# Optimization experiments

Measured on AMD Instinct MI355X. Metric: run time of the kernel, lower is better.

The kernel has to match this reference:

```python
import jax, jax.numpy as jnp
import numpy as np

N_QUBITS = 10
N_LAYERS = 4
DIM = 1 << N_QUBITS            # 1024
N3 = 3 * N_QUBITS              # params per rotation layer
N_PARAM = N3 * (N_LAYERS + 1)  # 150
BATCH = 8192

_C64 = jnp.complex64


def _rx(t):
    c = jnp.cos(t / 2).astype(_C64)
    s = jnp.sin(t / 2).astype(_C64)
    return jnp.stack([jnp.stack([c, -1j * s]), jnp.stack([-1j * s, c])])


def _ry(t):
    c = jnp.cos(t / 2).astype(_C64)
    s = jnp.sin(t / 2).astype(_C64)
    return jnp.stack([jnp.stack([c, -s]), jnp.stack([s, c])])


def _rz(t):
    e = jnp.exp(-1j * t.astype(_C64) / 2)
    z = jnp.zeros((), _C64)
    return jnp.stack([jnp.stack([e, z]), jnp.stack([z, jnp.conj(e)])])


def _apply1(state, gate, wire):
    """Apply a 2x2 gate to qubit `wire` of state [B, 2, ..., 2]."""
    axis = wire + 1  # axis 0 is batch
    s = jnp.moveaxis(state, axis, -1)
    s = jnp.einsum('ij,...j->...i', gate, s)
    return jnp.moveaxis(s, -1, axis)


def _cnot(state, ctrl, tgt):
    a, b = ctrl + 1, tgt + 1
    s = jnp.moveaxis(state, (a, b), (-2, -1))  # [..., ctrl, tgt]
    s = jnp.stack([s[..., 0, :], s[..., 1, ::-1]], axis=-2)
    return jnp.moveaxis(s, (-2, -1), (a, b))


def setup_inputs() -> dict:
    key = jax.random.key(0)
    k1, k2 = jax.random.split(key)
    x = jax.random.normal(k1, (BATCH, DIM), dtype=jnp.float32)
    he_std = (2.0 ** 0.5) * (5.0 ** -0.5)  # gain * 5^-0.5, w_mul with lrmul=1
    weight = jax.random.uniform(k2, (N_PARAM,), minval=0.0,
                                maxval=2.0 * np.pi, dtype=jnp.float32) * he_std
    return {"x": x, "weight": weight}


def reference(x, weight):
    # encoding layer: L2-normalize then cast to complex amplitudes
    norm = jnp.linalg.norm(x, axis=-1, keepdims=True)
    s = (x / jnp.maximum(norm, 1e-12)).astype(_C64)
    s = s.reshape((x.shape[0],) + (2,) * N_QUBITS)

    for l in range(N_LAYERS):
        w = weight[l * N3:(l + 1) * N3]
        # XYZ layer: Rx, then Ry, then Rz on every qubit
        for q in range(N_QUBITS):
            s = _apply1(s, _rx(w[q]), q)
        for q in range(N_QUBITS):
            s = _apply1(s, _ry(w[N_QUBITS + q]), q)
        for q in range(N_QUBITS):
            s = _apply1(s, _rz(w[2 * N_QUBITS + q]), q)
        # ring of CNOTs
        for q in range(N_QUBITS):
            s = _cnot(s, q, (q + 1) % N_QUBITS)

    # final YZY layer
    w = weight[N_LAYERS * N3:]
    for q in range(N_QUBITS):
        s = _apply1(s, _ry(w[q]), q)
    for q in range(N_QUBITS):
        s = _apply1(s, _rz(w[N_QUBITS + q]), q)
    for q in range(N_QUBITS):
        s = _apply1(s, _ry(w[2 * N_QUBITS + q]), q)

    return s.reshape(x.shape[0], 1, DIM).real
```

## Files before the change

kernel.cpp:

```cpp
#include <hip/hip_runtime.h>
#include <stdint.h>

typedef uint16_t u16;
typedef __attribute__((ext_vector_type(2))) float f32x2;
typedef __attribute__((ext_vector_type(4))) float f32x4;
typedef __attribute__((ext_vector_type(8))) short short8;
typedef __attribute__((ext_vector_type(4))) float float4v;
typedef __attribute__((ext_vector_type(4))) uint16_t u16x4;
typedef __attribute__((ext_vector_type(8))) uint16_t u16x8;

#define DIMQ 1024
#define BATCH 8192
#define KDIM 1024
#define NDIM 1024

#define RDL(v, l) __int_as_float(__builtin_amdgcn_readlane(__float_as_int(v), (l)))

__device__ __forceinline__ u16 f2bf(float f) {
  uint32_t u = __float_as_uint(f);
  u += 0x7fffu + ((u >> 16) & 1u);
  return (u16)(u >> 16);
}

template<int MASK>
__device__ __forceinline__ float lane_xor(float x) {
  if constexpr (MASK == 1)
    return __int_as_float(__builtin_amdgcn_update_dpp(0, __float_as_int(x), 0xB1, 0xF, 0xF, true));
  else if constexpr (MASK == 2)
    return __int_as_float(__builtin_amdgcn_update_dpp(0, __float_as_int(x), 0x4E, 0xF, 0xF, true));
  else if constexpr (MASK == 8)
    return __int_as_float(__builtin_amdgcn_update_dpp(0, __float_as_int(x), 0x128, 0xF, 0xF, true));
  else if constexpr (MASK == 4)
    return __int_as_float(__builtin_amdgcn_ds_swizzle(__float_as_int(x), 0x101F));
  else if constexpr (MASK == 16)
    return __int_as_float(__builtin_amdgcn_ds_swizzle(__float_as_int(x), 0x401F));
  else
    return __shfl_xor(x, 32, 64);
}

template<int MASK>
__device__ __forceinline__ void lane_gate8(float* ar, float* ai, int lane,
    float u00r, float u00i, float u01r, float u01i,
    float u10r, float u10i, float u11r, float u11i) {
  bool hi = (lane & MASK) != 0;
  float cmr = hi ? u11r : u00r, cmi = hi ? u11i : u00i;
  float cor = hi ? u10r : u01r, coi = hi ? u10i : u01i;
  float otr[8], oti[8];
#pragma unroll
  for (int r = 0; r < 8; ++r) otr[r] = lane_xor<MASK>(ar[r]);
#pragma unroll
  for (int r = 0; r < 8; ++r) oti[r] = lane_xor<MASK>(ai[r]);
#pragma unroll
  for (int k = 0; k < 4; ++k) {
    f32x2 A = {ar[2*k], ar[2*k+1]}, I = {ai[2*k], ai[2*k+1]};
    f32x2 R = {otr[2*k], otr[2*k+1]}, J = {oti[2*k], oti[2*k+1]};
    f32x2 nr = A*cmr - I*cmi + R*cor - J*coi;
    f32x2 ni = I*cmr + A*cmi + J*cor + R*coi;
    ar[2*k] = nr[0]; ar[2*k+1] = nr[1];
    ai[2*k] = ni[0]; ai[2*k+1] = ni[1];
  }
}

__device__ __forceinline__ void bfly2(f32x2 &a0r, f32x2 &a0i, f32x2 &a1r, f32x2 &a1i,
    float u00r, float u00i, float u01r, float u01i,
    float u10r, float u10i, float u11r, float u11i) {
  f32x2 t0r = a0r*u00r - a0i*u00i + a1r*u01r - a1i*u01i;
  f32x2 t0i = a0i*u00r + a0r*u00i + a1i*u01r + a1r*u01i;
  f32x2 t1r = a0r*u10r - a0i*u10i + a1r*u11r - a1i*u11i;
  f32x2 t1i = a0i*u10r + a0r*u10i + a1i*u11r + a1r*u11i;
  a0r = t0r; a0i = t0i; a1r = t1r; a1i = t1i;
}

__device__ inline void cmul2x2(float* O, const float* A, const float* B) {
  for (int r = 0; r < 2; ++r)
    for (int c = 0; c < 2; ++c) {
      float re = 0.f, im = 0.f;
      for (int j = 0; j < 2; ++j) {
        float ar = A[(r*2+j)*2], ai = A[(r*2+j)*2+1];
        float br = B[(j*2+c)*2], bi = B[(j*2+c)*2+1];
        re += ar*br - ai*bi;
        im += ar*bi + ai*br;
      }
      O[(r*2+c)*2]   = re;
      O[(r*2+c)*2+1] = im;
    }
}
__device__ inline void mk_rx(float* m, float t) {
  float s, c; sincosf(0.5f*t, &s, &c);
  m[0]=c; m[1]=0; m[2]=0; m[3]=-s; m[4]=0; m[5]=-s; m[6]=c; m[7]=0;
}
__device__ inline void mk_ry(float* m, float t) {
  float s, c; sincosf(0.5f*t, &s, &c);
  m[0]=c; m[1]=0; m[2]=-s; m[3]=0; m[4]=s; m[5]=0; m[6]=c; m[7]=0;
}
__device__ inline void mk_rz(float* m, float t) {
  float s, c; sincosf(0.5f*t, &s, &c);
  m[0]=c; m[1]=-s; m[2]=0; m[3]=0; m[4]=0; m[5]=0; m[6]=c; m[7]=s;
}

__device__ __forceinline__ int padi(int y) { return y + (y >> 4); }

__device__ __forceinline__ void do_stage(int gbase, float (&ar)[8], float (&ai)[8],
    f32x2* __restrict__ slab,
    const int (&Y)[8],
    int wbase, int lane, int h, int l4,
    float O0, float O1, float O2, float O3,
    float O4, float O5, float O6, float O7) {
#pragma unroll
  for (int j = 0; j < 8; ++j) slab[wbase + j] = (f32x2){ar[j], ai[j]};
  __syncthreads();
  {
    const int g6 = gbase + 6, g1 = gbase + 1;
    float u6r0 = h ? RDL(O4,g6) : RDL(O0,g6), u6i0 = h ? RDL(O5,g6) : RDL(O1,g6);
    float u6r1 = h ? RDL(O6,g6) : RDL(O2,g6), u6i1 = h ? RDL(O7,g6) : RDL(O3,g6);
    float u1r0 = l4 ? RDL(O4,g1) : RDL(O0,g1), u1i0 = l4 ? RDL(O5,g1) : RDL(O1,g1);
    float u1r1 = l4 ? RDL(O6,g1) : RDL(O2,g1), u1i1 = l4 ? RDL(O7,g1) : RDL(O3,g1);
    float KR[4], KI[4];
    KR[0] = u6r0*u1r0 - u6i0*u1i0;  KI[0] = u6r0*u1i0 + u6i0*u1r0;
    KR[1] = u6r0*u1r1 - u6i0*u1i1;  KI[1] = u6r0*u1i1 + u6i0*u1r1;
    KR[2] = u6r1*u1r0 - u6i1*u1i0;  KI[2] = u6r1*u1i0 + u6i1*u1r0;
    KR[3] = u6r1*u1r1 - u6i1*u1i1;  KI[3] = u6r1*u1i1 + u6i1*u1r1;
    const int CC[4] = {0, 1023, 527, 496};
    f32x2 v[8][4];
#pragma unroll
    for (int j = 0; j < 8; ++j)
#pragma unroll
      for (int m = 0; m < 4; ++m)
        v[j][m] = slab[padi(Y[j] ^ CC[m])];
#pragma unroll
    for (int k = 0; k < 4; ++k) {
      f32x2 nr = {0.f, 0.f}, ni = {0.f, 0.f};
#pragma unroll
      for (int m = 0; m < 4; ++m) {
        f32x2 Vr = {v[2*k][m][0], v[2*k+1][m][0]};
        f32x2 Vi = {v[2*k][m][1], v[2*k+1][m][1]};
        nr += Vr*KR[m] - Vi*KI[m];
        ni += Vi*KR[m] + Vr*KI[m];
      }
      ar[2*k] = nr[0]; ar[2*k+1] = nr[1];
      ai[2*k] = ni[0]; ai[2*k+1] = ni[1];
    }
  }
  { int g = gbase + 7;
    float u0r=RDL(O0,g),u0i=RDL(O1,g),u1r=RDL(O2,g),u1i=RDL(O3,g);
    float u2r=RDL(O4,g),u2i=RDL(O5,g),u3r=RDL(O6,g),u3i=RDL(O7,g);
    f32x2 a0r={ar[0],ar[1]}, a0i={ai[0],ai[1]}, a1r={ar[4],ar[5]}, a1i={ai[4],ai[5]};
    bfly2(a0r,a0i,a1r,a1i, u0r,u0i,u1r,u1i,u2r,u2i,u3r,u3i);
    ar[0]=a0r[0];ar[1]=a0r[1];ai[0]=a0i[0];ai[1]=a0i[1];
    ar[4]=a1r[0];ar[5]=a1r[1];ai[4]=a1i[0];ai[5]=a1i[1];
    f32x2 b0r={ar[2],ar[3]}, b0i={ai[2],ai[3]}, b1r={ar[6],ar[7]}, b1i={ai[6],ai[7]};
    bfly2(b0r,b0i,b1r,b1i, u0r,u0i,u1r,u1i,u2r,u2i,u3r,u3i);
    ar[2]=b0r[0];ar[3]=b0r[1];ai[2]=b0i[0];ai[3]=b0i[1];
    ar[6]=b1r[0];ar[7]=b1r[1];ai[6]=b1i[0];ai[7]=b1i[1];
  }
  { int g = gbase + 8;
    float u0r=RDL(O0,g),u0i=RDL(O1,g),u1r=RDL(O2,g),u1i=RDL(O3,g);
    float u2r=RDL(O4,g),u2i=RDL(O5,g),u3r=RDL(O6,g),u3i=RDL(O7,g);
    f32x2 a0r={ar[0],ar[1]}, a0i={ai[0],ai[1]}, a1r={ar[2],ar[3]}, a1i={ai[2],ai[3]};
    bfly2(a0r,a0i,a1r,a1i, u0r,u0i,u1r,u1i,u2r,u2i,u3r,u3i);
    ar[0]=a0r[0];ar[1]=a0r[1];ai[0]=a0i[0];ai[1]=a0i[1];
    ar[2]=a1r[0];ar[3]=a1r[1];ai[2]=a1i[0];ai[3]=a1i[1];
    f32x2 b0r={ar[4],ar[5]}, b0i={ai[4],ai[5]}, b1r={ar[6],ar[7]}, b1i={ai[6],ai[7]};
    bfly2(b0r,b0i,b1r,b1i, u0r,u0i,u1r,u1i,u2r,u2i,u3r,u3i);
    ar[4]=b0r[0];ar[5]=b0r[1];ai[4]=b0i[0];ai[5]=b0i[1];
    ar[6]=b1r[0];ar[7]=b1r[1];ai[6]=b1i[0];ai[7]=b1i[1];
  }
  { int g = gbase + 9;
    float u0r=RDL(O0,g),u0i=RDL(O1,g),u1r=RDL(O2,g),u1i=RDL(O3,g);
    float u2r=RDL(O4,g),u2i=RDL(O5,g),u3r=RDL(O6,g),u3i=RDL(O7,g);
    f32x2 a0r={ar[0],ar[2]}, a0i={ai[0],ai[2]}, a1r={ar[1],ar[3]}, a1i={ai[1],ai[3]};
    bfly2(a0r,a0i,a1r,a1i, u0r,u0i,u1r,u1i,u2r,u2i,u3r,u3i);
    ar[0]=a0r[0];ar[2]=a0r[1];ai[0]=a0i[0];ai[2]=a0i[1];
    ar[1]=a1r[0];ar[3]=a1r[1];ai[1]=a1i[0];ai[3]=a1i[1];
    f32x2 b0r={ar[4],ar[6]}, b0i={ai[4],ai[6]}, b1r={ar[5],ar[7]}, b1i={ai[5],ai[7]};
    bfly2(b0r,b0i,b1r,b1i, u0r,u0i,u1r,u1i,u2r,u2i,u3r,u3i);
    ar[4]=b0r[0];ar[6]=b0r[1];ai[4]=b0i[0];ai[6]=b0i[1];
    ar[5]=b1r[0];ar[7]=b1r[1];ai[5]=b1i[0];ai[7]=b1i[1];
  }
  { int g = gbase + 0; lane_gate8<32>(ar, ai, lane, RDL(O0,g),RDL(O1,g),RDL(O2,g),RDL(O3,g),RDL(O4,g),RDL(O5,g),RDL(O6,g),RDL(O7,g)); }
  { int g = gbase + 2; lane_gate8< 8>(ar, ai, lane, RDL(O0,g),RDL(O1,g),RDL(O2,g),RDL(O3,g),RDL(O4,g),RDL(O5,g),RDL(O6,g),RDL(O7,g)); }
  { int g = gbase + 3; lane_gate8< 4>(ar, ai, lane, RDL(O0,g),RDL(O1,g),RDL(O2,g),RDL(O3,g),RDL(O4,g),RDL(O5,g),RDL(O6,g),RDL(O7,g)); }
  { int g = gbase + 4; lane_gate8< 2>(ar, ai, lane, RDL(O0,g),RDL(O1,g),RDL(O2,g),RDL(O3,g),RDL(O4,g),RDL(O5,g),RDL(O6,g),RDL(O7,g)); }
  { int g = gbase + 5; lane_gate8< 1>(ar, ai, lane, RDL(O0,g),RDL(O1,g),RDL(O2,g),RDL(O3,g),RDL(O4,g),RDL(O5,g),RDL(O6,g),RDL(O7,g)); }
}

__global__ __launch_bounds__(256) void fused_front(const float* __restrict__ x,
                                                   const float* __restrict__ w,
                                                   u16* __restrict__ Abf,
                                                   u16* __restrict__ Bmat) {
  __shared__ f32x2 slab[2][2][1088];
  const int bid = blockIdx.x;
  const int lane = threadIdx.x & 63, wv = threadIdx.x >> 6;

  if (bid >= 512) {
    int base = (bid - 512) * 16 + wv * 4;
    for (int it = 0; it < 4; ++it) {
      int row = base + it;
      const float* xr = x + (size_t)row * DIMQ;
      float4v v[4];
      float ss = 0.f;
#pragma unroll
      for (int j = 0; j < 4; ++j) {
        v[j] = *(const float4v*)(xr + j*256 + lane*4);
        ss += v[j][0]*v[j][0] + v[j][1]*v[j][1] + v[j][2]*v[j][2] + v[j][3]*v[j][3];
      }
#pragma unroll
      for (int off = 32; off; off >>= 1) ss += __shfl_xor(ss, off, 64);
      float inv = 1.0f / fmaxf(sqrtf(ss), 1e-12f);
      u16* orow = Abf + (size_t)row * DIMQ;
#pragma unroll
      for (int j = 0; j < 4; ++j) {
        u16x4 o;
#pragma unroll
        for (int e = 0; e < 4; ++e) o[e] = f2bf(v[j][e] * inv);
        *(u16x4*)(orow + j*256 + lane*4) = o;
      }
    }
    return;
  }

  const int s = wv >> 1, h = wv & 1;
  const int l4 = (lane >> 4) & 1;
  const int d = bid * 2 + s;

  float O0, O1, O2, O3, O4, O5, O6, O7;
  {
    float A[8], B[8], C[8], T8[8], O[8];
    int t = lane;
    if (t < 50) {
      if (t < 10) {
        mk_ry(A, -w[120 + t]);
        mk_rz(B, -w[130 + t]);
        mk_ry(C, -w[140 + t]);
      } else {
        int sg = (t - 10) / 10, q = (t - 10) % 10, l = 3 - sg;
        mk_rx(A, -w[l*30 + q]);
        mk_ry(B, -w[l*30 + 10 + q]);
        mk_rz(C, -w[l*30 + 20 + q]);
      }
      cmul2x2(T8, A, B);
      cmul2x2(O, T8, C);
    } else {
#pragma unroll
      for (int j = 0; j < 8; ++j) O[j] = 0.f;
    }
    O0=O[0]; O1=O[1]; O2=O[2]; O3=O[3]; O4=O[4]; O5=O[5]; O6=O[6]; O7=O[7];
  }

  int Y[8];
#pragma unroll
  for (int j = 0; j < 8; ++j) {
    int xx = (lane << 4) + (h << 3) + j;
    int yy = xx;
#pragma unroll
    for (int qq = 0; qq < 9; ++qq) yy ^= ((yy >> (9 - qq)) & 1) << (8 - qq);
    yy ^= (yy & 1) << 9;
    Y[j] = yy ^ (h ? 527 : 0) ^ (l4 ? 1023 : 0);
  }
  const int wbase = lane * 17 + h * 8;

  float ar[8], ai[8];
  {
    float fr = 1.0f, fi = 0.0f;
#pragma unroll
    for (int p = 4; p <= 9; ++p) {
      const int q = 9 - p;
      int c = (d >> p) & 1;
      float a0r = c ? RDL(O2,q) : RDL(O0,q), a0i = c ? RDL(O3,q) : RDL(O1,q);
      float a1r = c ? RDL(O6,q) : RDL(O4,q), a1i = c ? RDL(O7,q) : RDL(O5,q);
      bool hb = (lane >> (p - 4)) & 1;
      float gr = hb ? a1r : a0r, gi = hb ? a1i : a0i;
      float nr = fr*gr - fi*gi, ni = fr*gi + fi*gr;
      fr = nr; fi = ni;
    }
    {
      int c = (d >> 3) & 1;
      float a0r = c ? RDL(O2,6) : RDL(O0,6), a0i = c ? RDL(O3,6) : RDL(O1,6);
      float a1r = c ? RDL(O6,6) : RDL(O4,6), a1i = c ? RDL(O7,6) : RDL(O5,6);
      float gr = h ? a1r : a0r, gi = h ? a1i : a0i;
      float nr = fr*gr - fi*gi, ni = fr*gi + fi*gr;
      fr = nr; fi = ni;
    }
    float t2r[2], t2i[2], t1r[2], t1i[2], t0r[2], t0i[2];
    {
      int c = (d >> 2) & 1;
      t2r[0] = c ? RDL(O2,7) : RDL(O0,7); t2i[0] = c ? RDL(O3,7) : RDL(O1,7);
      t2r[1] = c ? RDL(O6,7) : RDL(O4,7); t2i[1] = c ? RDL(O7,7) : RDL(O5,7);
    }
    {
      int c = (d >> 1) & 1;
      t1r[0] = c ? RDL(O2,8) : RDL(O0,8); t1i[0] = c ? RDL(O3,8) : RDL(O1,8);
      t1r[1] = c ? RDL(O6,8) : RDL(O4,8); t1i[1] = c ? RDL(O7,8) : RDL(O5,8);
    }
    {
      int c = d & 1;
      t0r[0] = c ? RDL(O2,9) : RDL(O0,9); t0i[0] = c ? RDL(O3,9) : RDL(O1,9);
      t0r[1] = c ? RDL(O6,9) : RDL(O4,9); t0i[1] = c ? RDL(O7,9) : RDL(O5,9);
    }
    float m21r[4], m21i[4];
#pragma unroll
    for (int b2 = 0; b2 < 2; ++b2)
#pragma unroll
      for (int b1 = 0; b1 < 2; ++b1) {
        m21r[b2*2+b1] = t2r[b2]*t1r[b1] - t2i[b2]*t1i[b1];
        m21i[b2*2+b1] = t2r[b2]*t1i[b1] + t2i[b2]*t1r[b1];
      }
#pragma unroll
    for (int j = 0; j < 8; ++j) {
      int hi2 = j >> 1;
      int b0 = j & 1;
      float wr = m21r[hi2]*t0r[b0] - m21i[hi2]*t0i[b0];
      float wi = m21r[hi2]*t0i[b0] + m21i[hi2]*t0r[b0];
      ar[j] = fr*wr - fi*wi;
      ai[j] = fr*wi + fi*wr;
    }
  }

  do_stage(10, ar, ai, slab[s][0], Y, wbase, lane, h, l4, O0,O1,O2,O3,O4,O5,O6,O7);
  do_stage(20, ar, ai, slab[s][1], Y, wbase, lane, h, l4, O0,O1,O2,O3,O4,O5,O6,O7);
  do_stage(30, ar, ai, slab[s][0], Y, wbase, lane, h, l4, O0,O1,O2,O3,O4,O5,O6,O7);
  do_stage(40, ar, ai, slab[s][1], Y, wbase, lane, h, l4, O0,O1,O2,O3,O4,O5,O6,O7);

  u16x8 o;
#pragma unroll
  for (int j = 0; j < 8; ++j) o[j] = f2bf(ar[j]);
  *(u16x8*)(Bmat + (size_t)d * DIMQ + lane*16 + h*8) = o;
}

__global__ __launch_bounds__(512) void gemm_bt(const u16* __restrict__ A,
                                               const u16* __restrict__ Bm,
                                               float* __restrict__ C) {
  __shared__ u16 As[3][256*64];
  __shared__ u16 Bs[3][128*64];
  const int t = threadIdx.x, lane = t & 63, wave = t >> 6;
  int bid = blockIdx.x;
  int nid = ((bid & 7) << 5) | (bid >> 3);
  const int bm = nid >> 3, bn = nid & 7;
  const size_t aBase = (size_t)bm * 256 * KDIM;
  const size_t bBase = (size_t)bn * 128 * KDIM;

  const int srow = t >> 3;
  const int scol = ((t & 7) ^ (srow & 7)) * 8;
  const int dstB = srow * 128 + (t & 7) * 16;

  const int wm = wave >> 2, wn = wave & 3;
  const int la = lane & 15;
  const int lkB = ((lane >> 4) * 16);
  const int rsw = (lane & 7) << 4;

  f32x4 acc[8][2];
#pragma unroll
  for (int m = 0; m < 8; ++m)
#pragma unroll
    for (int n = 0; n < 2; ++n) acc[m][n] = (f32x4){0.f, 0.f, 0.f, 0.f};

  auto stage = [&](int b, int kt) {
    int k0 = kt * 64;
#pragma unroll
    for (int j = 0; j < 4; ++j) {
      __builtin_amdgcn_global_load_lds(
          (const __attribute__((address_space(1))) void*)(A + aBase + (size_t)(j*64 + srow)*KDIM + k0 + scol),
          (__attribute__((address_space(3))) void*)((char*)&As[b][0] + j*8192 + dstB), 16, 0, 0);
    }
#pragma unroll
    for (int j = 0; j < 2; ++j) {
      __builtin_amdgcn_global_load_lds(
          (const __attribute__((address_space(1))) void*)(Bm + bBase + (size_t)(j*64 + srow)*KDIM + k0 + scol),
          (__attribute__((address_space(3))) void*)((char*)&Bs[b][0] + j*8192 + dstB), 16, 0, 0);
    }
  };

  stage(0, 0);
  stage(1, 1);

#pragma clang loop unroll(disable)
  for (int kt = 0; kt < 16; ++kt) {
    const int cur = kt % 3;
    if (kt < 15)
      asm volatile("s_waitcnt vmcnt(6)" ::: "memory");
    else
      asm volatile("s_waitcnt vmcnt(0)" ::: "memory");
    __builtin_amdgcn_s_barrier();
    short8 af[8][2], bf[2][2];
#pragma unroll
    for (int kk = 0; kk < 2; ++kk) {
#pragma unroll
      for (int m = 0; m < 8; ++m) {
        int row = wm*128 + m*16 + la;
        int byt = (row*128 + kk*64 + lkB) ^ rsw;
        af[m][kk] = *(const short8*)((char*)&As[cur][0] + byt);
      }
#pragma unroll
      for (int n = 0; n < 2; ++n) {
        int row = wn*32 + n*16 + la;
        int byt = (row*128 + kk*64 + lkB) ^ rsw;
        bf[n][kk] = *(const short8*)((char*)&Bs[cur][0] + byt);
      }
    }
    if (kt < 14) stage((kt + 2) % 3, kt + 2);
    __builtin_amdgcn_s_setprio(1);
#pragma unroll
    for (int kk = 0; kk < 2; ++kk)
#pragma unroll
      for (int m = 0; m < 8; ++m)
#pragma unroll
        for (int n = 0; n < 2; ++n)
          acc[m][n] = __builtin_amdgcn_mfma_f32_16x16x32_bf16(af[m][kk], bf[n][kk], acc[m][n], 0, 0, 0);
    __builtin_amdgcn_s_setprio(0);
  }

  int orow0 = bm*256 + wm*128 + (lane >> 4)*4;
  int ocol0 = bn*128 + wn*32 + la;
#pragma unroll
  for (int m = 0; m < 8; ++m)
#pragma unroll
    for (int n = 0; n < 2; ++n)
#pragma unroll
      for (int j = 0; j < 4; ++j)
        C[(size_t)(orow0 + m*16 + j)*NDIM + ocol0 + n*16] = acc[m][n][j];
}

extern "C" void kernel_launch(void* const* d_in, const int* in_sizes, int n_in,
                              void* d_out, int out_size, void* d_ws, size_t ws_size,
                              hipStream_t stream) {
  const float* x = (const float*)d_in[0];
  const float* w = (const float*)d_in[1];
  float* out = (float*)d_out;
  char* ws = (char*)d_ws;
  u16* Bmat = (u16*)(ws + 4096);
  u16* Abf  = (u16*)(ws + 4096 + 2*1024*1024);

  fused_front<<<1024, 256, 0, stream>>>(x, w, Abf, Bmat);
  gemm_bt<<<(BATCH/256)*(NDIM/128), 512, 0, stream>>>(Abf, Bmat, out);
}
```

Baseline: 48.08 us.

## Simulate one circuit column per wave with 16 amplitudes per lane, dropping block barriers

The circuit-matrix build used to split each 1024-amplitude state across two waves (8 amplitudes per lane) and exchanged data through shared memory with __syncthreads between stages. Now each wave owns a full column with 16 amplitudes per lane and its own private LDS slab, so no block barrier is needed. Qubit 0 now sits in the LDS permutation step rather than a cross-half lane shuffle, and the stage loop is kept rolled to limit code size. The circuit part needs half as many blocks. This raises register pressure and the per-lane LDS traffic per wave, and it depends on intra-wave ordering between LDS writes and reads being correct without an explicit barrier.

```diff
diff --git a/kernel.cpp b/kernel.cpp
--- a/kernel.cpp
+++ b/kernel.cpp
@@ -30,28 +30,24 @@
     return __int_as_float(__builtin_amdgcn_update_dpp(0, __float_as_int(x), 0x4E, 0xF, 0xF, true));
   else if constexpr (MASK == 8)
     return __int_as_float(__builtin_amdgcn_update_dpp(0, __float_as_int(x), 0x128, 0xF, 0xF, true));
-  else if constexpr (MASK == 4)
+  else
     return __int_as_float(__builtin_amdgcn_ds_swizzle(__float_as_int(x), 0x101F));
-  else if constexpr (MASK == 16)
-    return __int_as_float(__builtin_amdgcn_ds_swizzle(__float_as_int(x), 0x401F));
-  else
-    return __shfl_xor(x, 32, 64);
 }
 
 template<int MASK>
-__device__ __forceinline__ void lane_gate8(float* ar, float* ai, int lane,
+__device__ __forceinline__ void lane_gate16(float* ar, float* ai, int lane,
     float u00r, float u00i, float u01r, float u01i,
     float u10r, float u10i, float u11r, float u11i) {
   bool hi = (lane & MASK) != 0;
   float cmr = hi ? u11r : u00r, cmi = hi ? u11i : u00i;
   float cor = hi ? u10r : u01r, coi = hi ? u10i : u01i;
-  float otr[8], oti[8];
-#pragma unroll
-  for (int r = 0; r < 8; ++r) otr[r] = lane_xor<MASK>(ar[r]);
-#pragma unroll
-  for (int r = 0; r < 8; ++r) oti[r] = lane_xor<MASK>(ai[r]);
-#pragma unroll
-  for (int k = 0; k < 4; ++k) {
+  float otr[16], oti[16];
+#pragma unroll
+  for (int r = 0; r < 16; ++r) otr[r] = lane_xor<MASK>(ar[r]);
+#pragma unroll
+  for (int r = 0; r < 16; ++r) oti[r] = lane_xor<MASK>(ai[r]);
+#pragma unroll
+  for (int k = 0; k < 8; ++k) {
     f32x2 A = {ar[2*k], ar[2*k+1]}, I = {ai[2*k], ai[2*k+1]};
     f32x2 R = {otr[2*k], otr[2*k+1]}, J = {oti[2*k], oti[2*k+1]};
     f32x2 nr = A*cmr - I*cmi + R*cor - J*coi;
@@ -70,6 +66,20 @@
   f32x2 t1i = a0i*u10r + a0r*u10i + a1i*u11r + a1r*u11i;
   a0r = t0r; a0i = t0i; a1r = t1r; a1i = t1i;
 }
+
+#define BFLY2_ADJ(p0, p1, u0r,u0i,u1r,u1i,u2r,u2i,u3r,u3i)                 \
+  { f32x2 a0r={ar[p0],ar[p0+1]}, a0i={ai[p0],ai[p0+1]};                    \
+    f32x2 a1r={ar[p1],ar[p1+1]}, a1i={ai[p1],ai[p1+1]};                    \
+    bfly2(a0r,a0i,a1r,a1i, u0r,u0i,u1r,u1i,u2r,u2i,u3r,u3i);               \
+    ar[p0]=a0r[0];ar[p0+1]=a0r[1];ai[p0]=a0i[0];ai[p0+1]=a0i[1];           \
+    ar[p1]=a1r[0];ar[p1+1]=a1r[1];ai[p1]=a1i[0];ai[p1+1]=a1i[1]; }
+
+#define BFLY2_B0(p0, u0r,u0i,u1r,u1i,u2r,u2i,u3r,u3i)                      \
+  { f32x2 a0r={ar[p0],ar[p0+2]}, a0i={ai[p0],ai[p0+2]};                    \
+    f32x2 a1r={ar[p0+1],ar[p0+3]}, a1i={ai[p0+1],ai[p0+3]};                \
+    bfly2(a0r,a0i,a1r,a1i, u0r,u0i,u1r,u1i,u2r,u2i,u3r,u3i);               \
+    ar[p0]=a0r[0];ar[p0+2]=a0r[1];ai[p0]=a0i[0];ai[p0+2]=a0i[1];           \
+    ar[p0+1]=a1r[0];ar[p0+3]=a1r[1];ai[p0+1]=a1i[0];ai[p0+3]=a1i[1]; }
 
 __device__ inline void cmul2x2(float* O, const float* A, const float* B) {
   for (int r = 0; r < 2; ++r)
@@ -100,100 +110,16 @@
 
 __device__ __forceinline__ int padi(int y) { return y + (y >> 4); }
 
-__device__ __forceinline__ void do_stage(int gbase, float (&ar)[8], float (&ai)[8],
-    f32x2* __restrict__ slab,
-    const int (&Y)[8],
-    int wbase, int lane, int h, int l4,
-    float O0, float O1, float O2, float O3,
-    float O4, float O5, float O6, float O7) {
-#pragma unroll
-  for (int j = 0; j < 8; ++j) slab[wbase + j] = (f32x2){ar[j], ai[j]};
-  __syncthreads();
-  {
-    const int g6 = gbase + 6, g1 = gbase + 1;
-    float u6r0 = h ? RDL(O4,g6) : RDL(O0,g6), u6i0 = h ? RDL(O5,g6) : RDL(O1,g6);
-    float u6r1 = h ? RDL(O6,g6) : RDL(O2,g6), u6i1 = h ? RDL(O7,g6) : RDL(O3,g6);
-    float u1r0 = l4 ? RDL(O4,g1) : RDL(O0,g1), u1i0 = l4 ? RDL(O5,g1) : RDL(O1,g1);
-    float u1r1 = l4 ? RDL(O6,g1) : RDL(O2,g1), u1i1 = l4 ? RDL(O7,g1) : RDL(O3,g1);
-    float KR[4], KI[4];
-    KR[0] = u6r0*u1r0 - u6i0*u1i0;  KI[0] = u6r0*u1i0 + u6i0*u1r0;
-    KR[1] = u6r0*u1r1 - u6i0*u1i1;  KI[1] = u6r0*u1i1 + u6i0*u1r1;
-    KR[2] = u6r1*u1r0 - u6i1*u1i0;  KI[2] = u6r1*u1i0 + u6i1*u1r0;
-    KR[3] = u6r1*u1r1 - u6i1*u1i1;  KI[3] = u6r1*u1i1 + u6i1*u1r1;
-    const int CC[4] = {0, 1023, 527, 496};
-    f32x2 v[8][4];
-#pragma unroll
-    for (int j = 0; j < 8; ++j)
-#pragma unroll
-      for (int m = 0; m < 4; ++m)
-        v[j][m] = slab[padi(Y[j] ^ CC[m])];
-#pragma unroll
-    for (int k = 0; k < 4; ++k) {
-      f32x2 nr = {0.f, 0.f}, ni = {0.f, 0.f};
-#pragma unroll
-      for (int m = 0; m < 4; ++m) {
-        f32x2 Vr = {v[2*k][m][0], v[2*k+1][m][0]};
-        f32x2 Vi = {v[2*k][m][1], v[2*k+1][m][1]};
-        nr += Vr*KR[m] - Vi*KI[m];
-        ni += Vi*KR[m] + Vr*KI[m];
-      }
-      ar[2*k] = nr[0]; ar[2*k+1] = nr[1];
-      ai[2*k] = ni[0]; ai[2*k+1] = ni[1];
-    }
-  }
-  { int g = gbase + 7;
-    float u0r=RDL(O0,g),u0i=RDL(O1,g),u1r=RDL(O2,g),u1i=RDL(O3,g);
-    float u2r=RDL(O4,g),u2i=RDL(O5,g),u3r=RDL(O6,g),u3i=RDL(O7,g);
-    f32x2 a0r={ar[0],ar[1]}, a0i={ai[0],ai[1]}, a1r={ar[4],ar[5]}, a1i={ai[4],ai[5]};
-    bfly2(a0r,a0i,a1r,a1i, u0r,u0i,u1r,u1i,u2r,u2i,u3r,u3i);
-    ar[0]=a0r[0];ar[1]=a0r[1];ai[0]=a0i[0];ai[1]=a0i[1];
-    ar[4]=a1r[0];ar[5]=a1r[1];ai[4]=a1i[0];ai[5]=a1i[1];
-    f32x2 b0r={ar[2],ar[3]}, b0i={ai[2],ai[3]}, b1r={ar[6],ar[7]}, b1i={ai[6],ai[7]};
-    bfly2(b0r,b0i,b1r,b1i, u0r,u0i,u1r,u1i,u2r,u2i,u3r,u3i);
-    ar[2]=b0r[0];ar[3]=b0r[1];ai[2]=b0i[0];ai[3]=b0i[1];
-    ar[6]=b1r[0];ar[7]=b1r[1];ai[6]=b1i[0];ai[7]=b1i[1];
-  }
-  { int g = gbase + 8;
-    float u0r=RDL(O0,g),u0i=RDL(O1,g),u1r=RDL(O2,g),u1i=RDL(O3,g);
-    float u2r=RDL(O4,g),u2i=RDL(O5,g),u3r=RDL(O6,g),u3i=RDL(O7,g);
-    f32x2 a0r={ar[0],ar[1]}, a0i={ai[0],ai[1]}, a1r={ar[2],ar[3]}, a1i={ai[2],ai[3]};
-    bfly2(a0r,a0i,a1r,a1i, u0r,u0i,u1r,u1i,u2r,u2i,u3r,u3i);
-    ar[0]=a0r[0];ar[1]=a0r[1];ai[0]=a0i[0];ai[1]=a0i[1];
-    ar[2]=a1r[0];ar[3]=a1r[1];ai[2]=a1i[0];ai[3]=a1i[1];
-    f32x2 b0r={ar[4],ar[5]}, b0i={ai[4],ai[5]}, b1r={ar[6],ar[7]}, b1i={ai[6],ai[7]};
-    bfly2(b0r,b0i,b1r,b1i, u0r,u0i,u1r,u1i,u2r,u2i,u3r,u3i);
-    ar[4]=b0r[0];ar[5]=b0r[1];ai[4]=b0i[0];ai[5]=b0i[1];
-    ar[6]=b1r[0];ar[7]=b1r[1];ai[6]=b1i[0];ai[7]=b1i[1];
-  }
-  { int g = gbase + 9;
-    float u0r=RDL(O0,g),u0i=RDL(O1,g),u1r=RDL(O2,g),u1i=RDL(O3,g);
-    float u2r=RDL(O4,g),u2i=RDL(O5,g),u3r=RDL(O6,g),u3i=RDL(O7,g);
-    f32x2 a0r={ar[0],ar[2]}, a0i={ai[0],ai[2]}, a1r={ar[1],ar[3]}, a1i={ai[1],ai[3]};
-    bfly2(a0r,a0i,a1r,a1i, u0r,u0i,u1r,u1i,u2r,u2i,u3r,u3i);
-    ar[0]=a0r[0];ar[2]=a0r[1];ai[0]=a0i[0];ai[2]=a0i[1];
-    ar[1]=a1r[0];ar[3]=a1r[1];ai[1]=a1i[0];ai[3]=a1i[1];
-    f32x2 b0r={ar[4],ar[6]}, b0i={ai[4],ai[6]}, b1r={ar[5],ar[7]}, b1i={ai[5],ai[7]};
-    bfly2(b0r,b0i,b1r,b1i, u0r,u0i,u1r,u1i,u2r,u2i,u3r,u3i);
-    ar[4]=b0r[0];ar[6]=b0r[1];ai[4]=b0i[0];ai[6]=b0i[1];
-    ar[5]=b1r[0];ar[7]=b1r[1];ai[5]=b1i[0];ai[7]=b1i[1];
-  }
-  { int g = gbase + 0; lane_gate8<32>(ar, ai, lane, RDL(O0,g),RDL(O1,g),RDL(O2,g),RDL(O3,g),RDL(O4,g),RDL(O5,g),RDL(O6,g),RDL(O7,g)); }
-  { int g = gbase + 2; lane_gate8< 8>(ar, ai, lane, RDL(O0,g),RDL(O1,g),RDL(O2,g),RDL(O3,g),RDL(O4,g),RDL(O5,g),RDL(O6,g),RDL(O7,g)); }
-  { int g = gbase + 3; lane_gate8< 4>(ar, ai, lane, RDL(O0,g),RDL(O1,g),RDL(O2,g),RDL(O3,g),RDL(O4,g),RDL(O5,g),RDL(O6,g),RDL(O7,g)); }
-  { int g = gbase + 4; lane_gate8< 2>(ar, ai, lane, RDL(O0,g),RDL(O1,g),RDL(O2,g),RDL(O3,g),RDL(O4,g),RDL(O5,g),RDL(O6,g),RDL(O7,g)); }
-  { int g = gbase + 5; lane_gate8< 1>(ar, ai, lane, RDL(O0,g),RDL(O1,g),RDL(O2,g),RDL(O3,g),RDL(O4,g),RDL(O5,g),RDL(O6,g),RDL(O7,g)); }
-}
-
 __global__ __launch_bounds__(256) void fused_front(const float* __restrict__ x,
                                                    const float* __restrict__ w,
                                                    u16* __restrict__ Abf,
                                                    u16* __restrict__ Bmat) {
-  __shared__ f32x2 slab[2][2][1088];
+  __shared__ f32x2 slab4[4][1088];
   const int bid = blockIdx.x;
   const int lane = threadIdx.x & 63, wv = threadIdx.x >> 6;
 
-  if (bid >= 512) {
-    int base = (bid - 512) * 16 + wv * 4;
+  if (bid >= 256) {
+    int base = (bid - 256) * 16 + wv * 4;
     for (int it = 0; it < 4; ++it) {
       int row = base + it;
       const float* xr = x + (size_t)row * DIMQ;
@@ -219,9 +145,9 @@
     return;
   }
 
-  const int s = wv >> 1, h = wv & 1;
-  const int l4 = (lane >> 4) & 1;
-  const int d = bid * 2 + s;
+  f32x2* __restrict__ slab = slab4[wv];
+  const int d = bid * 4 + wv;
+  const int l5 = lane >> 5, l4 = (lane >> 4) & 1;
 
   float O0, O1, O2, O3, O4, O5, O6, O7;
   {
@@ -247,19 +173,19 @@
     O0=O[0]; O1=O[1]; O2=O[2]; O3=O[3]; O4=O[4]; O5=O[5]; O6=O[6]; O7=O[7];
   }
 
-  int Y[8];
-#pragma unroll
-  for (int j = 0; j < 8; ++j) {
-    int xx = (lane << 4) + (h << 3) + j;
+  int Y[16];
+#pragma unroll
+  for (int j = 0; j < 16; ++j) {
+    int xx = (lane << 4) + j;
     int yy = xx;
 #pragma unroll
     for (int qq = 0; qq < 9; ++qq) yy ^= ((yy >> (9 - qq)) & 1) << (8 - qq);
     yy ^= (yy & 1) << 9;
-    Y[j] = yy ^ (h ? 527 : 0) ^ (l4 ? 1023 : 0);
-  }
-  const int wbase = lane * 17 + h * 8;
-
-  float ar[8], ai[8];
+    Y[j] = yy ^ (l5 ? 511 : 0) ^ (l4 ? 1023 : 0);
+  }
+  const int wbase = lane * 17;
+
+  float ar[16], ai[16];
   {
     float fr = 1.0f, fi = 0.0f;
 #pragma unroll
@@ -273,58 +199,129 @@
       float nr = fr*gr - fi*gi, ni = fr*gi + fi*gr;
       fr = nr; fi = ni;
     }
-    {
-      int c = (d >> 3) & 1;
-      float a0r = c ? RDL(O2,6) : RDL(O0,6), a0i = c ? RDL(O3,6) : RDL(O1,6);
-      float a1r = c ? RDL(O6,6) : RDL(O4,6), a1i = c ? RDL(O7,6) : RDL(O5,6);
-      float gr = h ? a1r : a0r, gi = h ? a1i : a0i;
-      float nr = fr*gr - fi*gi, ni = fr*gi + fi*gr;
-      fr = nr; fi = ni;
-    }
-    float t2r[2], t2i[2], t1r[2], t1i[2], t0r[2], t0i[2];
-    {
-      int c = (d >> 2) & 1;
+    float t3r[2], t3i[2], t2r[2], t2i[2], t1r[2], t1i[2], t0r[2], t0i[2];
+    { int c = (d >> 3) & 1;
+      t3r[0] = c ? RDL(O2,6) : RDL(O0,6); t3i[0] = c ? RDL(O3,6) : RDL(O1,6);
+      t3r[1] = c ? RDL(O6,6) : RDL(O4,6); t3i[1] = c ? RDL(O7,6) : RDL(O5,6); }
+    { int c = (d >> 2) & 1;
       t2r[0] = c ? RDL(O2,7) : RDL(O0,7); t2i[0] = c ? RDL(O3,7) : RDL(O1,7);
-      t2r[1] = c ? RDL(O6,7) : RDL(O4,7); t2i[1] = c ? RDL(O7,7) : RDL(O5,7);
-    }
-    {
-      int c = (d >> 1) & 1;
+      t2r[1] = c ? RDL(O6,7) : RDL(O4,7); t2i[1] = c ? RDL(O7,7) : RDL(O5,7); }
+    { int c = (d >> 1) & 1;
       t1r[0] = c ? RDL(O2,8) : RDL(O0,8); t1i[0] = c ? RDL(O3,8) : RDL(O1,8);
-      t1r[1] = c ? RDL(O6,8) : RDL(O4,8); t1i[1] = c ? RDL(O7,8) : RDL(O5,8);
-    }
-    {
-      int c = d & 1;
+      t1r[1] = c ? RDL(O6,8) : RDL(O4,8); t1i[1] = c ? RDL(O7,8) : RDL(O5,8); }
+    { int c = d & 1;
       t0r[0] = c ? RDL(O2,9) : RDL(O0,9); t0i[0] = c ? RDL(O3,9) : RDL(O1,9);
-      t0r[1] = c ? RDL(O6,9) : RDL(O4,9); t0i[1] = c ? RDL(O7,9) : RDL(O5,9);
-    }
-    float m21r[4], m21i[4];
-#pragma unroll
-    for (int b2 = 0; b2 < 2; ++b2)
-#pragma unroll
-      for (int b1 = 0; b1 < 2; ++b1) {
-        m21r[b2*2+b1] = t2r[b2]*t1r[b1] - t2i[b2]*t1i[b1];
-        m21i[b2*2+b1] = t2r[b2]*t1i[b1] + t2i[b2]*t1r[b1];
-      }
-#pragma unroll
-    for (int j = 0; j < 8; ++j) {
-      int hi2 = j >> 1;
-      int b0 = j & 1;
-      float wr = m21r[hi2]*t0r[b0] - m21i[hi2]*t0i[b0];
-      float wi = m21r[hi2]*t0i[b0] + m21i[hi2]*t0r[b0];
-      ar[j] = fr*wr - fi*wi;
-      ai[j] = fr*wi + fi*wr;
-    }
-  }
-
-  do_stage(10, ar, ai, slab[s][0], Y, wbase, lane, h, l4, O0,O1,O2,O3,O4,O5,O6,O7);
-  do_stage(20, ar, ai, slab[s][1], Y, wbase, lane, h, l4, O0,O1,O2,O3,O4,O5,O6,O7);
-  do_stage(30, ar, ai, slab[s][0], Y, wbase, lane, h, l4, O0,O1,O2,O3,O4,O5,O6,O7);
-  do_stage(40, ar, ai, slab[s][1], Y, wbase, lane, h, l4, O0,O1,O2,O3,O4,O5,O6,O7);
-
-  u16x8 o;
-#pragma unroll
-  for (int j = 0; j < 8; ++j) o[j] = f2bf(ar[j]);
-  *(u16x8*)(Bmat + (size_t)d * DIMQ + lane*16 + h*8) = o;
+      t0r[1] = c ? RDL(O6,9) : RDL(O4,9); t0i[1] = c ? RDL(O7,9) : RDL(O5,9); }
+    float m32r[4], m32i[4], m10r[4], m10i[4];
+#pragma unroll
+    for (int b3 = 0; b3 < 2; ++b3)
+#pragma unroll
+      for (int b2 = 0; b2 < 2; ++b2) {
+        m32r[b3*2+b2] = t3r[b3]*t2r[b2] - t3i[b3]*t2i[b2];
+        m32i[b3*2+b2] = t3r[b3]*t2i[b2] + t3i[b3]*t2r[b2];
+      }
+#pragma unroll
+    for (int b1 = 0; b1 < 2; ++b1)
+#pragma unroll
+      for (int b0 = 0; b0 < 2; ++b0) {
+        m10r[b1*2+b0] = t1r[b1]*t0r[b0] - t1i[b1]*t0i[b0];
+        m10i[b1*2+b0] = t1r[b1]*t0i[b0] + t1i[b1]*t0r[b0];
+      }
+#pragma unroll
+    for (int j = 0; j < 16; ++j) {
+      int hi2 = j >> 2, lo2 = j & 3;
+      float mr = m32r[hi2]*m10r[lo2] - m32i[hi2]*m10i[lo2];
+      float mi = m32r[hi2]*m10i[lo2] + m32i[hi2]*m10r[lo2];
+      ar[j] = fr*mr - fi*mi;
+      ai[j] = fr*mi + fi*mr;
+    }
+  }
+
+#pragma clang loop unroll(disable)
+  for (int stage = 1; stage < 5; ++stage) {
+    const int gbase = stage * 10;
+#pragma unroll
+    for (int j = 0; j < 16; ++j) slab[wbase + j] = (f32x2){ar[j], ai[j]};
+    const int g0 = gbase + 0, g1 = gbase + 1;
+    float u0r0 = l5 ? RDL(O4,g0) : RDL(O0,g0), u0i0 = l5 ? RDL(O5,g0) : RDL(O1,g0);
+    float u0r1 = l5 ? RDL(O6,g0) : RDL(O2,g0), u0i1 = l5 ? RDL(O7,g0) : RDL(O3,g0);
+    float u1r0 = l4 ? RDL(O4,g1) : RDL(O0,g1), u1i0 = l4 ? RDL(O5,g1) : RDL(O1,g1);
+    float u1r1 = l4 ? RDL(O6,g1) : RDL(O2,g1), u1i1 = l4 ? RDL(O7,g1) : RDL(O3,g1);
+    float KR[4], KI[4];
+    KR[0] = u0r0*u1r0 - u0i0*u1i0;  KI[0] = u0r0*u1i0 + u0i0*u1r0;
+    KR[1] = u0r0*u1r1 - u0i0*u1i1;  KI[1] = u0r0*u1i1 + u0i0*u1r1;
+    KR[2] = u0r1*u1r0 - u0i1*u1i0;  KI[2] = u0r1*u1i0 + u0i1*u1r0;
+    KR[3] = u0r1*u1r1 - u0i1*u1i1;  KI[3] = u0r1*u1i1 + u0i1*u1r1;
+    const int CC[4] = {0, 1023, 511, 512};
+#pragma unroll
+    for (int hf = 0; hf < 2; ++hf) {
+      float nr[8], ni[8];
+#pragma unroll
+      for (int k = 0; k < 8; ++k) { nr[k] = 0.f; ni[k] = 0.f; }
+#pragma unroll
+      for (int m = 0; m < 4; ++m) {
+        f32x2 v[8];
+#pragma unroll
+        for (int k = 0; k < 8; ++k) v[k] = slab[padi(Y[hf*8 + k] ^ CC[m])];
+#pragma unroll
+        for (int k = 0; k < 4; ++k) {
+          f32x2 Vr = {v[2*k][0], v[2*k+1][0]};
+          f32x2 Vi = {v[2*k][1], v[2*k+1][1]};
+          f32x2 pr = Vr*KR[m] - Vi*KI[m];
+          f32x2 pi = Vi*KR[m] + Vr*KI[m];
+          nr[2*k] += pr[0]; nr[2*k+1] += pr[1];
+          ni[2*k] += pi[0]; ni[2*k+1] += pi[1];
+        }
+      }
+#pragma unroll
+      for (int k = 0; k < 8; ++k) { ar[hf*8 + k] = nr[k]; ai[hf*8 + k] = ni[k]; }
+    }
+    { int g = gbase + 6;
+      float u0r=RDL(O0,g),u0i=RDL(O1,g),u1r=RDL(O2,g),u1i=RDL(O3,g);
+      float u2r=RDL(O4,g),u2i=RDL(O5,g),u3r=RDL(O6,g),u3i=RDL(O7,g);
+      BFLY2_ADJ(0, 8,  u0r,u0i,u1r,u1i,u2r,u2i,u3r,u3i);
+      BFLY2_ADJ(2, 10, u0r,u0i,u1r,u1i,u2r,u2i,u3r,u3i);
+      BFLY2_ADJ(4, 12, u0r,u0i,u1r,u1i,u2r,u2i,u3r,u3i);
+      BFLY2_ADJ(6, 14, u0r,u0i,u1r,u1i,u2r,u2i,u3r,u3i);
+    }
+    { int g = gbase + 7;
+      float u0r=RDL(O0,g),u0i=RDL(O1,g),u1r=RDL(O2,g),u1i=RDL(O3,g);
+      float u2r=RDL(O4,g),u2i=RDL(O5,g),u3r=RDL(O6,g),u3i=RDL(O7,g);
+      BFLY2_ADJ(0, 4,  u0r,u0i,u1r,u1i,u2r,u2i,u3r,u3i);
+      BFLY2_ADJ(2, 6,  u0r,u0i,u1r,u1i,u2r,u2i,u3r,u3i);
+      BFLY2_ADJ(8, 12, u0r,u0i,u1r,u1i,u2r,u2i,u3r,u3i);
+      BFLY2_ADJ(10,14, u0r,u0i,u1r,u1i,u2r,u2i,u3r,u3i);
+    }
+    { int g = gbase + 8;
+      float u0r=RDL(O0,g),u0i=RDL(O1,g),u1r=RDL(O2,g),u1i=RDL(O3,g);
+      float u2r=RDL(O4,g),u2i=RDL(O5,g),u3r=RDL(O6,g),u3i=RDL(O7,g);
+      BFLY2_ADJ(0, 2,  u0r,u0i,u1r,u1i,u2r,u2i,u3r,u3i);
+      BFLY2_ADJ(4, 6,  u0r,u0i,u1r,u1i,u2r,u2i,u3r,u3i);
+      BFLY2_ADJ(8, 10, u0r,u0i,u1r,u1i,u2r,u2i,u3r,u3i);
+      BFLY2_ADJ(12,14, u0r,u0i,u1r,u1i,u2r,u2i,u3r,u3i);
+    }
+    { int g = gbase + 9;
+      float u0r=RDL(O0,g),u0i=RDL(O1,g),u1r=RDL(O2,g),u1i=RDL(O3,g);
+      float u2r=RDL(O4,g),u2i=RDL(O5,g),u3r=RDL(O6,g),u3i=RDL(O7,g);
+      BFLY2_B0(0,  u0r,u0i,u1r,u1i,u2r,u2i,u3r,u3i);
+      BFLY2_B0(4,  u0r,u0i,u1r,u1i,u2r,u2i,u3r,u3i);
+      BFLY2_B0(8,  u0r,u0i,u1r,u1i,u2r,u2i,u3r,u3i);
+      BFLY2_B0(12, u0r,u0i,u1r,u1i,u2r,u2i,u3r,u3i);
+    }
+    { int g = gbase + 2; lane_gate16<8>(ar, ai, lane, RDL(O0,g),RDL(O1,g),RDL(O2,g),RDL(O3,g),RDL(O4,g),RDL(O5,g),RDL(O6,g),RDL(O7,g)); }
+    { int g = gbase + 3; lane_gate16<4>(ar, ai, lane, RDL(O0,g),RDL(O1,g),RDL(O2,g),RDL(O3,g),RDL(O4,g),RDL(O5,g),RDL(O6,g),RDL(O7,g)); }
+    { int g = gbase + 4; lane_gate16<2>(ar, ai, lane, RDL(O0,g),RDL(O1,g),RDL(O2,g),RDL(O3,g),RDL(O4,g),RDL(O5,g),RDL(O6,g),RDL(O7,g)); }
+    { int g = gbase + 5; lane_gate16<1>(ar, ai, lane, RDL(O0,g),RDL(O1,g),RDL(O2,g),RDL(O3,g),RDL(O4,g),RDL(O5,g),RDL(O6,g),RDL(O7,g)); }
+  }
+
+  u16x8 o0, o1;
+#pragma unroll
+  for (int j = 0; j < 8; ++j) o0[j] = f2bf(ar[j]);
+#pragma unroll
+  for (int j = 0; j < 8; ++j) o1[j] = f2bf(ar[8 + j]);
+  u16* row = Bmat + (size_t)d * DIMQ + lane * 16;
+  *(u16x8*)row = o0;
+  *(u16x8*)(row + 8) = o1;
 }
 
 __global__ __launch_bounds__(512) void gemm_bt(const u16* __restrict__ A,
@@ -430,6 +427,6 @@
   u16* Bmat = (u16*)(ws + 4096);
   u16* Abf  = (u16*)(ws + 4096 + 2*1024*1024);
 
-  fused_front<<<1024, 256, 0, stream>>>(x, w, Abf, Bmat);
+  fused_front<<<256 + 512, 256, 0, stream>>>(x, w, Abf, Bmat);
   gemm_bt<<<(BATCH/256)*(NDIM/128), 512, 0, stream>>>(Abf, Bmat, out);
 }
```

After: 48.33 us. About the same (+0.5%).
